# Optimization experiments

Hardware: AMD Instinct MI355X
Metric: run time of the kernel (lower is better)

## Reference

```python
import jax, jax.numpy as jnp
import numpy as np

DIM = 128
B, LQ, LK = 8, 2048, 2048


def setup_inputs() -> dict:
    key = jax.random.key(0)
    k1, k2, k3 = jax.random.split(key, 3)
    output = jax.random.normal(k1, (B, LQ, DIM), dtype=jnp.float32)
    context = jax.random.normal(k2, (B, LK, DIM), dtype=jnp.float32)
    mask = jax.random.randint(k3, (B, LQ, LK), 0, 2).astype(jnp.bool_)
    return {"output": output, "context": context, "mask": mask}


def reference(output, context, mask):
    temperature = jnp.asarray(np.power(DIM, 0.5), dtype=output.dtype)
    # scores: [B, Lq, Lk]
    attn = jnp.einsum('bqd,bkd->bqk', output, context) / temperature
    attn = jnp.where(mask, -jnp.inf, attn)
    out_attn = jax.nn.log_softmax(attn, axis=-1)
    p = jax.nn.softmax(attn, axis=-1)
    # dropout is identity in eval/reference mode
    out = jnp.einsum('bqk,bkd->bqd', p, context)
    return (out, out_attn)
```

## Files before the change

kernel.cpp:

```cpp
#include <hip/hip_runtime.h>
#include <cstdint>


#define DIMV 128
constexpr int BB = 8;
constexpr int LQ = 2048;
constexpr int LK = 2048;
constexpr float RTEMP = 0.08838834764831843f;

typedef _Float16 half8 __attribute__((ext_vector_type(8)));
typedef _Float16 half4v __attribute__((ext_vector_type(4)));
typedef float float4v __attribute__((ext_vector_type(4)));

__global__ __launch_bounds__(256) void prep_kernel(const float* __restrict__ q,
                                                   const float* __restrict__ ctx,
                                                   _Float16* __restrict__ Qf,
                                                   _Float16* __restrict__ Kf,
                                                   _Float16* __restrict__ Vf) {
    __shared__ float tile[32][132];
    const int tid  = threadIdx.x;
    const int mode = blockIdx.x >> 9;
    const int t    = blockIdx.x & 511;
    const int b    = t >> 6;
    const int r0   = (t & 63) * 32;
    const float4* s4 = (const float4*)((mode == 0 ? q : ctx) + ((size_t)b * 2048 + r0) * DIMV);
    for (int v = 0; v < 4; v++) {
        int off = tid + v * 256;
        float4 f = s4[off];
        int row = off >> 5, c4 = (off & 31) * 4;
        tile[row][c4 + 0] = f.x; tile[row][c4 + 1] = f.y;
        tile[row][c4 + 2] = f.z; tile[row][c4 + 3] = f.w;
    }
    __syncthreads();
    if (mode < 2) {
        _Float16* dst = (mode == 0 ? Qf : Kf) + (size_t)b * (2048 * DIMV);
        for (int c = 0; c < 2; c++) {
            int chunk = tid + c * 256;
            int t2 = chunk >> 8, kk = (chunk >> 6) & 3, lane = chunk & 63;
            int quad = lane >> 4, l16 = lane & 15;
            int r = t2 * 16 + l16, d0 = kk * 32 + quad * 8;
            half8 h;
            for (int e = 0; e < 8; e++) h[e] = (_Float16)tile[r][d0 + e];
            size_t tl = (size_t)(r0 >> 4) + t2;
            *(half8*)(dst + ((tl * 4 + kk) * 64 + lane) * 8) = h;
        }
    } else {
        _Float16* dst = Vf + (size_t)b * (2048 * DIMV);
        const int kt0 = r0 >> 4;
        for (int c = 0; c < 2; c++) {
            int chunk = tid + c * 256;
            int ktl = chunk >> 8, dp = (chunk >> 6) & 3, ln = chunk & 63;
            int qd = ln >> 4, s16 = ln & 15;
            half8 h;
            for (int e = 0; e < 4; e++) {
                h[e]     = (_Float16)tile[ktl * 16 + qd * 4 + e][(2 * dp) * 16 + s16];
                h[e + 4] = (_Float16)tile[ktl * 16 + qd * 4 + e][(2 * dp + 1) * 16 + s16];
            }
            *(half8*)(dst + ((((size_t)(kt0 + ktl)) * 4 + dp) * 64 + ln) * 8) = h;
        }
    }
}

__global__ __launch_bounds__(256, 4)
void attn_kernel(const unsigned char* __restrict__ mask,
                 const _Float16* __restrict__ Qf, const _Float16* __restrict__ Kf,
                 const _Float16* __restrict__ Vf,
                 float* __restrict__ out, float* __restrict__ out_attn) {
    constexpr int TQ = 16;
    __shared__ __attribute__((aligned(16))) float pvred[4][TQ][132];
    __shared__ float redm[4][TQ];
    __shared__ float redl[4][TQ];
    __shared__ float swf[4][TQ];
    __shared__ float mcl[TQ];
    __shared__ float rls[TQ];

    const int tid  = threadIdx.x;
    const int wave = tid >> 6;
    const int lane = tid & 63;
    const int l16  = lane & 15;
    const int quad = lane >> 4;

    const int b  = blockIdx.x & 7;
    const int qt = blockIdx.x >> 3;
    const int q0 = qt * TQ;

    const _Float16* Qb = Qf + (size_t)b * (2048 * DIMV);
    const _Float16* Kb = Kf + (size_t)b * (2048 * DIMV);
    const _Float16* Vb = Vf + (size_t)b * (2048 * DIMV);

    half8 qfrag[4];
#pragma unroll
    for (int kk = 0; kk < 4; kk++)
        qfrag[kk] = *(const half8*)(Qb + (((size_t)qt * 4 + kk) * 64 + lane) * 8);

    const unsigned char* mrow = mask + ((size_t)b * LQ + q0 + l16) * LK + wave * 512 + quad * 4;

    const _Float16* kbase = Kb + (size_t)wave * 32 * 2048;
    const _Float16* vbase = Vb + (size_t)wave * 32 * 2048;

    const float NEGINF = -__builtin_inff();
    float m = -1e30f;
    float l = 0.f;
    float4v oacc[8];
#pragma unroll
    for (int dt = 0; dt < 8; dt++) oacc[dt] = (float4v){0.f, 0.f, 0.f, 0.f};

    for (int ct = 0; ct < 32; ct++) {
        const _Float16* kp = kbase + (size_t)ct * 2048;
        float4v st = (float4v){0.f, 0.f, 0.f, 0.f};
#pragma unroll
        for (int kk = 0; kk < 4; kk++) {
            half8 kf = *(const half8*)(kp + (kk * 64 + lane) * 8);
            st = __builtin_amdgcn_mfma_f32_16x16x32_f16(kf, qfrag[kk], st, 0, 0, 0);
        }
        const uint32_t mv = *(const uint32_t*)(mrow + ct * 16);
        float sv[4];
#pragma unroll
        for (int r = 0; r < 4; r++) {
            float v = st[r] * RTEMP;
            if ((mv >> (8 * r)) & 0xffu) v = NEGINF;
            sv[r] = v;
        }
        float tmax = fmaxf(fmaxf(sv[0], sv[1]), fmaxf(sv[2], sv[3]));
        tmax = fmaxf(tmax, __shfl_xor(tmax, 16));
        tmax = fmaxf(tmax, __shfl_xor(tmax, 32));
        const bool upd = tmax > m + 3.0f;
        if (__any(upd)) {
            const float mnew = upd ? tmax : m;
            const float sc = __expf(m - mnew);
            float scr[4];
#pragma unroll
            for (int r = 0; r < 4; r++) scr[r] = __shfl(sc, quad * 4 + r);
            l *= sc;
#pragma unroll
            for (int dt = 0; dt < 8; dt++)
#pragma unroll
                for (int r = 0; r < 4; r++) oacc[dt][r] *= scr[r];
            m = mnew;
        }
        half4v pa;
        float psum = 0.f;
#pragma unroll
        for (int r = 0; r < 4; r++) {
            const float p = __expf(sv[r] - m);
            psum += p;
            pa[r] = (_Float16)p;
        }
        psum += __shfl_xor(psum, 16);
        psum += __shfl_xor(psum, 32);
        l += psum;
        const _Float16* vp = vbase + (size_t)ct * 2048;
#pragma unroll
        for (int dp = 0; dp < 4; dp++) {
            half8 v8 = *(const half8*)(vp + (dp * 64 + lane) * 8);
            half4v vlo = __builtin_shufflevector(v8, v8, 0, 1, 2, 3);
            half4v vhi = __builtin_shufflevector(v8, v8, 4, 5, 6, 7);
            oacc[2 * dp]     = __builtin_amdgcn_mfma_f32_16x16x16f16(pa, vlo, oacc[2 * dp],     0, 0, 0);
            oacc[2 * dp + 1] = __builtin_amdgcn_mfma_f32_16x16x16f16(pa, vhi, oacc[2 * dp + 1], 0, 0, 0);
        }
    }

    if (quad == 0) { redm[wave][l16] = m; redl[wave][l16] = l; }
    __syncthreads();
    if (tid < TQ) {
        const float m0 = redm[0][tid], m1 = redm[1][tid], m2 = redm[2][tid], m3 = redm[3][tid];
        const float M = fmaxf(fmaxf(m0, m1), fmaxf(m2, m3));
        const float e0 = __expf(m0 - M), e1 = __expf(m1 - M);
        const float e2 = __expf(m2 - M), e3 = __expf(m3 - M);
        const float L = e0 * redl[0][tid] + e1 * redl[1][tid]
                      + e2 * redl[2][tid] + e3 * redl[3][tid];
        swf[0][tid] = e0; swf[1][tid] = e1; swf[2][tid] = e2; swf[3][tid] = e3;
        mcl[tid] = M + __logf(L);
        rls[tid] = 1.0f / L;
    }
    __syncthreads();

#pragma unroll
    for (int r = 0; r < 4; r++) {
        const float sc = swf[wave][quad * 4 + r];
#pragma unroll
        for (int dt = 0; dt < 8; dt++)
            pvred[wave][quad * 4 + r][dt * 16 + l16] = oacc[dt][r] * sc;
    }

    const float mc = mcl[l16];
    float* oa = out_attn + ((size_t)b * LQ + q0 + l16) * LK + wave * 512 + quad * 4;
#pragma unroll 2
    for (int ct = 0; ct < 32; ct++) {
        const _Float16* kp = kbase + (size_t)ct * 2048;
        float4v st = (float4v){0.f, 0.f, 0.f, 0.f};
#pragma unroll
        for (int kk = 0; kk < 4; kk++) {
            half8 kf = *(const half8*)(kp + (kk * 64 + lane) * 8);
            st = __builtin_amdgcn_mfma_f32_16x16x32_f16(kf, qfrag[kk], st, 0, 0, 0);
        }
        const uint32_t mv = *(const uint32_t*)(mrow + ct * 16);
        float4v o;
#pragma unroll
        for (int r = 0; r < 4; r++) {
            float logp = st[r] * RTEMP - mc;
            if ((mv >> (8 * r)) & 0xffu) logp = -1.0e30f;
            o[r] = fmaxf(logp, -1.0e30f);
        }
        *(float4v*)(oa + ct * 16) = o;
    }
    __syncthreads();

    {
        const int row = tid >> 4;
        const int c0 = (tid & 15) * 8;
        const float rcl = rls[row];
        float* op = out + ((size_t)b * LQ + q0 + row) * DIMV + c0;
#pragma unroll
        for (int h = 0; h < 2; h++) {
            const int c = c0 + h * 4;
            float4v a0 = *(const float4v*)&pvred[0][row][c];
            float4v a1 = *(const float4v*)&pvred[1][row][c];
            float4v a2 = *(const float4v*)&pvred[2][row][c];
            float4v a3 = *(const float4v*)&pvred[3][row][c];
            float4v v;
#pragma unroll
            for (int j = 0; j < 4; j++)
                v[j] = (a0[j] + a1[j] + a2[j] + a3[j]) * rcl;
            *(float4v*)(op + h * 4) = v;
        }
    }
}

extern "C" void kernel_launch(void* const* d_in, const int* in_sizes, int n_in,
                              void* d_out, int out_size, void* d_ws, size_t ws_size,
                              hipStream_t stream) {
    const float* q_f32 = (const float*)d_in[0];
    const float* c_f32 = (const float*)d_in[1];
    const unsigned char* mask = (const unsigned char*)d_in[2];

    float* out      = (float*)d_out;
    float* out_attn = out + (size_t)BB * LQ * DIMV;

    _Float16* Qf = (_Float16*)d_ws;
    _Float16* Kf = Qf + (size_t)BB * LQ * DIMV;
    _Float16* Vf = Kf + (size_t)BB * LK * DIMV;

    prep_kernel<<<1536, 256, 0, stream>>>(q_f32, c_f32, Qf, Kf, Vf);
    attn_kernel<<<BB * (LQ / 16), 256, 0, stream>>>(mask, Qf, Kf, Vf, out, out_attn);
}
```

Before: 298.1 us.

## Stage K/V tiles in LDS with double buffering, 64-query blocks of 8 waves

Each block now handles 64 query rows with 8 waves. K/V tiles are loaded cooperatively into double-buffered shared memory and shared across the two query groups, so each wave reuses K/V fragments for two 16-row subtiles instead of reading them directly from global memory. The 1/sqrt(d) scale is folded into Q during prep, which removes a multiply per score. The cost is a per-iteration block barrier, a larger LDS footprint (about 98KB) and launch_bounds(512,1), which may limit occupancy, plus a serialized 4-round reduction of partial outputs.

```diff
diff --git a/kernel.cpp b/kernel.cpp
--- a/kernel.cpp
+++ b/kernel.cpp
@@ -6,7 +6,7 @@
 constexpr int BB = 8;
 constexpr int LQ = 2048;
 constexpr int LK = 2048;
-constexpr float RTEMP = 0.08838834764831843f;
+constexpr float QSCALE = 0.08838834764831843f;
 
 typedef _Float16 half8 __attribute__((ext_vector_type(8)));
 typedef _Float16 half4v __attribute__((ext_vector_type(4)));
@@ -33,6 +33,7 @@
     }
     __syncthreads();
     if (mode < 2) {
+        const float qs = (mode == 0) ? QSCALE : 1.0f;
         _Float16* dst = (mode == 0 ? Qf : Kf) + (size_t)b * (2048 * DIMV);
         for (int c = 0; c < 2; c++) {
             int chunk = tid + c * 256;
@@ -40,7 +41,7 @@
             int quad = lane >> 4, l16 = lane & 15;
             int r = t2 * 16 + l16, d0 = kk * 32 + quad * 8;
             half8 h;
-            for (int e = 0; e < 8; e++) h[e] = (_Float16)tile[r][d0 + e];
+            for (int e = 0; e < 8; e++) h[e] = (_Float16)(tile[r][d0 + e] * qs);
             size_t tl = (size_t)(r0 >> 4) + t2;
             *(half8*)(dst + ((tl * 4 + kk) * 64 + lane) * 8) = h;
         }
@@ -61,169 +62,255 @@
     }
 }
 
-__global__ __launch_bounds__(256, 4)
+__global__ __launch_bounds__(512, 1)
 void attn_kernel(const unsigned char* __restrict__ mask,
                  const _Float16* __restrict__ Qf, const _Float16* __restrict__ Kf,
                  const _Float16* __restrict__ Vf,
                  float* __restrict__ out, float* __restrict__ out_attn) {
-    constexpr int TQ = 16;
-    __shared__ __attribute__((aligned(16))) float pvred[4][TQ][132];
-    __shared__ float redm[4][TQ];
-    __shared__ float redl[4][TQ];
-    __shared__ float swf[4][TQ];
-    __shared__ float mcl[TQ];
-    __shared__ float rls[TQ];
+    __shared__ __attribute__((aligned(16))) _Float16 STG[2][16384];
+    __shared__ __attribute__((aligned(16))) float pvsum[64][132];
+    __shared__ float redm[8][32], redl[8][32], swf[8][32];
+    __shared__ float mcl64[64], rls64[64];
 
     const int tid  = threadIdx.x;
     const int wave = tid >> 6;
     const int lane = tid & 63;
     const int l16  = lane & 15;
     const int quad = lane >> 4;
-
-    const int b  = blockIdx.x & 7;
-    const int qt = blockIdx.x >> 3;
-    const int q0 = qt * TQ;
+    const int p    = wave & 3;
+    const int qg   = wave >> 2;
+
+    const int b   = blockIdx.x & 7;
+    const int qt4 = blockIdx.x >> 3;
+    const int q0  = qt4 * 64;
 
     const _Float16* Qb = Qf + (size_t)b * (2048 * DIMV);
     const _Float16* Kb = Kf + (size_t)b * (2048 * DIMV);
     const _Float16* Vb = Vf + (size_t)b * (2048 * DIMV);
 
-    half8 qfrag[4];
-#pragma unroll
-    for (int kk = 0; kk < 4; kk++)
-        qfrag[kk] = *(const half8*)(Qb + (((size_t)qt * 4 + kk) * 64 + lane) * 8);
-
-    const unsigned char* mrow = mask + ((size_t)b * LQ + q0 + l16) * LK + wave * 512 + quad * 4;
-
-    const _Float16* kbase = Kb + (size_t)wave * 32 * 2048;
-    const _Float16* vbase = Vb + (size_t)wave * 32 * 2048;
+    half8 qfrag[2][4];
+#pragma unroll
+    for (int sub = 0; sub < 2; sub++) {
+        const size_t tq = (size_t)qt4 * 4 + qg * 2 + sub;
+#pragma unroll
+        for (int kk = 0; kk < 4; kk++)
+            qfrag[sub][kk] = *(const half8*)(Qb + ((tq * 4 + kk) * 64 + lane) * 8);
+    }
+
+    const unsigned char* mrow0 = mask + ((size_t)b * LQ + q0 + qg * 32 + l16) * LK + p * 16 + quad * 4;
 
     const float NEGINF = -__builtin_inff();
-    float m = -1e30f;
-    float l = 0.f;
-    float4v oacc[8];
-#pragma unroll
-    for (int dt = 0; dt < 8; dt++) oacc[dt] = (float4v){0.f, 0.f, 0.f, 0.f};
-
-    for (int ct = 0; ct < 32; ct++) {
-        const _Float16* kp = kbase + (size_t)ct * 2048;
-        float4v st = (float4v){0.f, 0.f, 0.f, 0.f};
-#pragma unroll
-        for (int kk = 0; kk < 4; kk++) {
-            half8 kf = *(const half8*)(kp + (kk * 64 + lane) * 8);
-            st = __builtin_amdgcn_mfma_f32_16x16x32_f16(kf, qfrag[kk], st, 0, 0, 0);
-        }
-        const uint32_t mv = *(const uint32_t*)(mrow + ct * 16);
-        float sv[4];
-#pragma unroll
-        for (int r = 0; r < 4; r++) {
-            float v = st[r] * RTEMP;
-            if ((mv >> (8 * r)) & 0xffu) v = NEGINF;
-            sv[r] = v;
-        }
-        float tmax = fmaxf(fmaxf(sv[0], sv[1]), fmaxf(sv[2], sv[3]));
-        tmax = fmaxf(tmax, __shfl_xor(tmax, 16));
-        tmax = fmaxf(tmax, __shfl_xor(tmax, 32));
-        const bool upd = tmax > m + 3.0f;
-        if (__any(upd)) {
-            const float mnew = upd ? tmax : m;
-            const float sc = __expf(m - mnew);
-            float scr[4];
-#pragma unroll
-            for (int r = 0; r < 4; r++) scr[r] = __shfl(sc, quad * 4 + r);
-            l *= sc;
-#pragma unroll
-            for (int dt = 0; dt < 8; dt++)
-#pragma unroll
-                for (int r = 0; r < 4; r++) oacc[dt][r] *= scr[r];
-            m = mnew;
-        }
-        half4v pa;
-        float psum = 0.f;
-#pragma unroll
-        for (int r = 0; r < 4; r++) {
-            const float p = __expf(sv[r] - m);
-            psum += p;
-            pa[r] = (_Float16)p;
-        }
-        psum += __shfl_xor(psum, 16);
-        psum += __shfl_xor(psum, 32);
-        l += psum;
-        const _Float16* vp = vbase + (size_t)ct * 2048;
-#pragma unroll
-        for (int dp = 0; dp < 4; dp++) {
-            half8 v8 = *(const half8*)(vp + (dp * 64 + lane) * 8);
-            half4v vlo = __builtin_shufflevector(v8, v8, 0, 1, 2, 3);
-            half4v vhi = __builtin_shufflevector(v8, v8, 4, 5, 6, 7);
-            oacc[2 * dp]     = __builtin_amdgcn_mfma_f32_16x16x16f16(pa, vlo, oacc[2 * dp],     0, 0, 0);
-            oacc[2 * dp + 1] = __builtin_amdgcn_mfma_f32_16x16x16f16(pa, vhi, oacc[2 * dp + 1], 0, 0, 0);
-        }
-    }
-
-    if (quad == 0) { redm[wave][l16] = m; redl[wave][l16] = l; }
-    __syncthreads();
-    if (tid < TQ) {
-        const float m0 = redm[0][tid], m1 = redm[1][tid], m2 = redm[2][tid], m3 = redm[3][tid];
-        const float M = fmaxf(fmaxf(m0, m1), fmaxf(m2, m3));
-        const float e0 = __expf(m0 - M), e1 = __expf(m1 - M);
-        const float e2 = __expf(m2 - M), e3 = __expf(m3 - M);
-        const float L = e0 * redl[0][tid] + e1 * redl[1][tid]
-                      + e2 * redl[2][tid] + e3 * redl[3][tid];
-        swf[0][tid] = e0; swf[1][tid] = e1; swf[2][tid] = e2; swf[3][tid] = e3;
-        mcl[tid] = M + __logf(L);
-        rls[tid] = 1.0f / L;
-    }
-    __syncthreads();
-
-#pragma unroll
-    for (int r = 0; r < 4; r++) {
-        const float sc = swf[wave][quad * 4 + r];
-#pragma unroll
-        for (int dt = 0; dt < 8; dt++)
-            pvred[wave][quad * 4 + r][dt * 16 + l16] = oacc[dt][r] * sc;
-    }
-
-    const float mc = mcl[l16];
-    float* oa = out_attn + ((size_t)b * LQ + q0 + l16) * LK + wave * 512 + quad * 4;
-#pragma unroll 2
-    for (int ct = 0; ct < 32; ct++) {
-        const _Float16* kp = kbase + (size_t)ct * 2048;
-        float4v st = (float4v){0.f, 0.f, 0.f, 0.f};
-#pragma unroll
-        for (int kk = 0; kk < 4; kk++) {
-            half8 kf = *(const half8*)(kp + (kk * 64 + lane) * 8);
-            st = __builtin_amdgcn_mfma_f32_16x16x32_f16(kf, qfrag[kk], st, 0, 0, 0);
-        }
-        const uint32_t mv = *(const uint32_t*)(mrow + ct * 16);
-        float4v o;
-#pragma unroll
-        for (int r = 0; r < 4; r++) {
-            float logp = st[r] * RTEMP - mc;
-            if ((mv >> (8 * r)) & 0xffu) logp = -1.0e30f;
-            o[r] = fmaxf(logp, -1.0e30f);
-        }
-        *(float4v*)(oa + ct * 16) = o;
-    }
-    __syncthreads();
+    float m0r = -1e30f, m1r = -1e30f;
+    float l0r = 0.f, l1r = 0.f;
+    float4v oacc[2][8];
+#pragma unroll
+    for (int sub = 0; sub < 2; sub++)
+#pragma unroll
+        for (int dt = 0; dt < 8; dt++) oacc[sub][dt] = (float4v){0.f, 0.f, 0.f, 0.f};
+
+    const _Float16* gsb = (wave < 4) ? Kb : Vb;
+    const int wt = wave & 3;
+    const unsigned dsto = ((wave < 4) ? 0u : 8192u) + (unsigned)wt * 2048;
 
     {
-        const int row = tid >> 4;
-        const int c0 = (tid & 15) * 8;
-        const float rcl = rls[row];
+        const _Float16* src = gsb + (size_t)(0 * 4 + wt) * 2048 + lane * 8;
+        float4 r4[4];
+#pragma unroll
+        for (int c = 0; c < 4; c++) r4[c] = *(const float4*)(src + c * 512);
+        _Float16* d = &STG[0][dsto];
+#pragma unroll
+        for (int c = 0; c < 4; c++) *(float4*)(d + c * 512 + lane * 8) = r4[c];
+    }
+    __syncthreads();
+
+    for (int i = 0; i < 32; ++i) {
+        const int cur = i & 1, nxt = cur ^ 1;
+        const bool more = (i + 1 < 32);
+        float4 nr4[4];
+        if (more) {
+            const _Float16* src = gsb + (size_t)(4 * (i + 1) + wt) * 2048 + lane * 8;
+#pragma unroll
+            for (int c = 0; c < 4; c++) nr4[c] = *(const float4*)(src + c * 512);
+        }
+
+        const _Float16* kt = &STG[cur][p * 2048];
+        const _Float16* vt = &STG[cur][8192 + p * 2048];
+        half8 kf[4], vv[4];
+#pragma unroll
+        for (int kk = 0; kk < 4; kk++) kf[kk] = *(const half8*)(kt + kk * 512 + lane * 8);
+#pragma unroll
+        for (int dp = 0; dp < 4; dp++) vv[dp] = *(const half8*)(vt + dp * 512 + lane * 8);
+
+#pragma unroll
+        for (int sub = 0; sub < 2; sub++) {
+            float4v st = (float4v){0.f, 0.f, 0.f, 0.f};
+#pragma unroll
+            for (int kk = 0; kk < 4; kk++)
+                st = __builtin_amdgcn_mfma_f32_16x16x32_f16(kf[kk], qfrag[sub][kk], st, 0, 0, 0);
+            const uint32_t mv = *(const uint32_t*)(mrow0 + (size_t)sub * 16 * LK + (size_t)i * 64);
+            float& m = sub ? m1r : m0r;
+            float& l = sub ? l1r : l0r;
+            float sv[4];
+#pragma unroll
+            for (int r = 0; r < 4; r++) {
+                float v = st[r];
+                if ((mv >> (8 * r)) & 0xffu) v = NEGINF;
+                sv[r] = v;
+            }
+            float tmax = fmaxf(fmaxf(sv[0], sv[1]), fmaxf(sv[2], sv[3]));
+            tmax = fmaxf(tmax, __shfl_xor(tmax, 16));
+            tmax = fmaxf(tmax, __shfl_xor(tmax, 32));
+            const bool upd = tmax > m + 3.0f;
+            if (__any(upd)) {
+                const float mnew = upd ? tmax : m;
+                const float sc = __expf(m - mnew);
+                float scr[4];
+#pragma unroll
+                for (int r = 0; r < 4; r++) scr[r] = __shfl(sc, quad * 4 + r);
+                l *= sc;
+#pragma unroll
+                for (int dt = 0; dt < 8; dt++)
+#pragma unroll
+                    for (int r = 0; r < 4; r++) oacc[sub][dt][r] *= scr[r];
+                m = mnew;
+            }
+            half4v pa;
+            float psum = 0.f;
+#pragma unroll
+            for (int r = 0; r < 4; r++) {
+                const float pp = __expf(sv[r] - m);
+                psum += pp;
+                pa[r] = (_Float16)pp;
+            }
+            psum += __shfl_xor(psum, 16);
+            psum += __shfl_xor(psum, 32);
+            l += psum;
+#pragma unroll
+            for (int dp = 0; dp < 4; dp++) {
+                half4v vlo = __builtin_shufflevector(vv[dp], vv[dp], 0, 1, 2, 3);
+                half4v vhi = __builtin_shufflevector(vv[dp], vv[dp], 4, 5, 6, 7);
+                oacc[sub][2 * dp]     = __builtin_amdgcn_mfma_f32_16x16x16f16(pa, vlo, oacc[sub][2 * dp],     0, 0, 0);
+                oacc[sub][2 * dp + 1] = __builtin_amdgcn_mfma_f32_16x16x16f16(pa, vhi, oacc[sub][2 * dp + 1], 0, 0, 0);
+            }
+        }
+
+        if (more) {
+            _Float16* d = &STG[nxt][dsto];
+#pragma unroll
+            for (int c = 0; c < 4; c++) *(float4*)(d + c * 512 + lane * 8) = nr4[c];
+        }
+        __syncthreads();
+    }
+
+    if (quad == 0) {
+        redm[wave][l16]      = m0r;  redm[wave][16 + l16] = m1r;
+        redl[wave][l16]      = l0r;  redl[wave][16 + l16] = l1r;
+    }
+    float4 pre2[2];
+    {
+        const int t0 = wave >> 2, kkw = wave & 3;
+        pre2[0] = *(const float4*)(Kb + (size_t)(t0)     * 2048 + kkw * 512 + lane * 8);
+        pre2[1] = *(const float4*)(Kb + (size_t)(t0 + 2) * 2048 + kkw * 512 + lane * 8);
+    }
+    __syncthreads();
+    if (tid < 64) {
+        const int qg2 = tid >> 5, r32 = tid & 31;
+        float mm[4], ll[4];
+#pragma unroll
+        for (int pp = 0; pp < 4; pp++) { mm[pp] = redm[qg2 * 4 + pp][r32]; ll[pp] = redl[qg2 * 4 + pp][r32]; }
+        const float M = fmaxf(fmaxf(mm[0], mm[1]), fmaxf(mm[2], mm[3]));
+        float L = 0.f;
+#pragma unroll
+        for (int pp = 0; pp < 4; pp++) {
+            const float e = __expf(mm[pp] - M);
+            swf[qg2 * 4 + pp][r32] = e;
+            L += e * ll[pp];
+        }
+        mcl64[tid] = M + __logf(L);
+        rls64[tid] = 1.0f / L;
+    }
+    __syncthreads();
+
+    for (int rnd = 0; rnd < 4; ++rnd) {
+        if (p == rnd) {
+#pragma unroll
+            for (int sub = 0; sub < 2; sub++)
+#pragma unroll
+                for (int r = 0; r < 4; r++) {
+                    const int row = qg * 32 + sub * 16 + quad * 4 + r;
+                    const float sc = swf[wave][sub * 16 + quad * 4 + r];
+#pragma unroll
+                    for (int dt = 0; dt < 8; dt++) {
+                        const float v = oacc[sub][dt][r] * sc;
+                        if (rnd == 0) pvsum[row][dt * 16 + l16] = v;
+                        else          pvsum[row][dt * 16 + l16] += v;
+                    }
+                }
+        }
+        __syncthreads();
+    }
+
+    {
+        const int row = tid >> 3;
+        const int c0  = (tid & 7) * 16;
+        const float rcl = rls64[row];
         float* op = out + ((size_t)b * LQ + q0 + row) * DIMV + c0;
 #pragma unroll
-        for (int h = 0; h < 2; h++) {
-            const int c = c0 + h * 4;
-            float4v a0 = *(const float4v*)&pvred[0][row][c];
-            float4v a1 = *(const float4v*)&pvred[1][row][c];
-            float4v a2 = *(const float4v*)&pvred[2][row][c];
-            float4v a3 = *(const float4v*)&pvred[3][row][c];
+        for (int h = 0; h < 4; h++) {
+            float4v a = *(const float4v*)&pvsum[row][c0 + h * 4];
             float4v v;
 #pragma unroll
-            for (int j = 0; j < 4; j++)
-                v[j] = (a0[j] + a1[j] + a2[j] + a3[j]) * rcl;
+            for (int j = 0; j < 4; j++) v[j] = a[j] * rcl;
             *(float4v*)(op + h * 4) = v;
         }
+    }
+
+    {
+        const int t0 = wave >> 2, kkw = wave & 3;
+        *(float4*)(&STG[0][(t0)     * 2048 + kkw * 512] + lane * 8) = pre2[0];
+        *(float4*)(&STG[0][(t0 + 2) * 2048 + kkw * 512] + lane * 8) = pre2[1];
+    }
+    __syncthreads();
+
+    const float mc0 = mcl64[qg * 32 + l16];
+    const float mc1 = mcl64[qg * 32 + 16 + l16];
+    float* oa0 = out_attn + ((size_t)b * LQ + q0 + qg * 32 + l16) * LK + p * 16 + quad * 4;
+    for (int i = 0; i < 32; ++i) {
+        const int cur = i & 1, nxt = cur ^ 1;
+        const bool more = (i + 1 < 32);
+        float4 n2[2];
+        if (more) {
+            const int t0 = wave >> 2, kkw = wave & 3;
+            n2[0] = *(const float4*)(Kb + (size_t)(4 * (i + 1) + t0)     * 2048 + kkw * 512 + lane * 8);
+            n2[1] = *(const float4*)(Kb + (size_t)(4 * (i + 1) + t0 + 2) * 2048 + kkw * 512 + lane * 8);
+        }
+        const _Float16* kt = &STG[cur][p * 2048];
+        half8 kf[4];
+#pragma unroll
+        for (int kk = 0; kk < 4; kk++) kf[kk] = *(const half8*)(kt + kk * 512 + lane * 8);
+#pragma unroll
+        for (int sub = 0; sub < 2; sub++) {
+            float4v st = (float4v){0.f, 0.f, 0.f, 0.f};
+#pragma unroll
+            for (int kk = 0; kk < 4; kk++)
+                st = __builtin_amdgcn_mfma_f32_16x16x32_f16(kf[kk], qfrag[sub][kk], st, 0, 0, 0);
+            const uint32_t mv = *(const uint32_t*)(mrow0 + (size_t)sub * 16 * LK + (size_t)i * 64);
+            const float mc = sub ? mc1 : mc0;
+            float4v o;
+#pragma unroll
+            for (int r = 0; r < 4; r++) {
+                float lp = st[r] - mc;
+                if ((mv >> (8 * r)) & 0xffu) lp = -1.0e30f;
+                o[r] = fmaxf(lp, -1.0e30f);
+            }
+            *(float4v*)(oa0 + (size_t)sub * 16 * LK + (size_t)i * 64) = o;
+        }
+        if (more) {
+            const int t0 = wave >> 2, kkw = wave & 3;
+            *(float4*)(&STG[nxt][(t0)     * 2048 + kkw * 512] + lane * 8) = n2[0];
+            *(float4*)(&STG[nxt][(t0 + 2) * 2048 + kkw * 512] + lane * 8) = n2[1];
+        }
+        __syncthreads();
     }
 }
 
@@ -242,5 +329,5 @@
     _Float16* Vf = Kf + (size_t)BB * LK * DIMV;
 
     prep_kernel<<<1536, 256, 0, stream>>>(q_f32, c_f32, Qf, Kf, Vf);
-    attn_kernel<<<BB * (LQ / 16), 256, 0, stream>>>(mask, Qf, Kf, Vf, out, out_attn);
+    attn_kernel<<<BB * (LQ / 64), 512, 0, stream>>>(mask, Qf, Kf, Vf, out, out_attn);
 }
```

New measurement: 304.0 us. 1.02x slower.
